# Kernel optimization log

Hardware: AMD Instinct MI355X
Metric: run time of the kernel (lower is better)

## Reference

```python
import jax, jax.numpy as jnp
import numpy as np

HEADS = 8
DIM_HEAD = 64
DIM = 128
TOPK = (8, 8, 8)  # depth, height, width


def chan_ln(x, g, b):
    # channel layernorm over axis=1 (biased variance), eps added to std
    mean = jnp.mean(x, axis=1, keepdims=True)
    var = jnp.var(x, axis=1, keepdims=True)
    return g * (x - mean) / (jnp.sqrt(var) + 1e-6) + b


def l2norm(x):
    # F.normalize(dim=1): divide by max(||x||_2, eps)
    n = jnp.sqrt(jnp.sum(x * x, axis=1, keepdims=True))
    return x / jnp.maximum(n, 1e-12)


def _forward(query_source, context, w_q, w_kv, w_out,
             ctx_gamma, ctx_beta, qs_gamma, qs_beta, out_gamma, out_beta, gamma):
    b, c, Dq, Hq, Wq = query_source.shape
    Dc, Hc, Wc = context.shape[2:]
    kd, kh, kw = TOPK

    ctx = chan_ln(context, ctx_gamma, ctx_beta)
    qs = chan_ln(query_source, qs_gamma, qs_beta)

    # 1x1x1 convs == channel matmuls
    kv = jnp.einsum('bcdhw,oc->bodhw', ctx, w_kv)   # (b, 2*inner, D, H, W)
    k, v = jnp.split(kv, 2, axis=1)
    q = jnp.einsum('bcdhw,oc->bodhw', qs, w_q)      # (b, inner, D, H, W)

    def fold(t):  # (b, h*c, D,H,W) -> (b*h, c, D,H,W)
        return t.reshape(b * HEADS, DIM_HEAD, *t.shape[2:])

    q, k, v = fold(q), fold(k), fold(v)
    q, k = l2norm(q), l2norm(k)

    q_probe = jnp.sum(q, axis=(2, 3, 4))            # (bh, c)
    k_abs = jnp.abs(k)

    if kd < Dc:
        score = jnp.einsum('bc,bcd->bd', q_probe, jnp.sum(k_abs, axis=(3, 4)))
        idx = jax.lax.top_k(score, kd)[1][:, None, :, None, None]
        k = jnp.take_along_axis(k, idx, axis=2)
        v = jnp.take_along_axis(v, idx, axis=2)
    if kh < Hc:
        score = jnp.einsum('bc,bch->bh', q_probe, jnp.sum(k_abs, axis=(2, 4)))
        idx = jax.lax.top_k(score, kh)[1][:, None, None, :, None]
        k = jnp.take_along_axis(k, idx, axis=3)
        v = jnp.take_along_axis(v, idx, axis=3)
    if kw < Wc:
        score = jnp.einsum('bc,bcw->bw', q_probe, jnp.sum(k_abs, axis=(2, 3)))
        idx = jax.lax.top_k(score, kw)[1][:, None, None, None, :]
        k = jnp.take_along_axis(k, idx, axis=4)
        v = jnp.take_along_axis(v, idx, axis=4)

    def flat(t):  # (bh, c, d, h, w) -> (bh, d*h*w, c)
        return t.reshape(t.shape[0], t.shape[1], -1).transpose(0, 2, 1)

    qf, kf, vf = flat(q), flat(k), flat(v)
    sim = jnp.einsum('bic,bjc->bij', qf, kf)        # (bh, Nq, Nkv)
    attn = jax.nn.softmax(sim, axis=-1)
    out = jnp.einsum('bij,bjc->bic', attn, vf)      # (bh, Nq, c)

    out = out.reshape(b, HEADS, Dq, Hq, Wq, DIM_HEAD)
    out = out.transpose(0, 1, 5, 2, 3, 4).reshape(b, HEADS * DIM_HEAD, Dq, Hq, Wq)
    out = jnp.einsum('bcdhw,oc->bodhw', out, w_out)
    out = chan_ln(out, out_gamma, out_beta)
    return gamma * out + query_source


def setup_inputs() -> dict:
    key = jax.random.key(0)
    ks = jax.random.split(key, 6)
    b, c, D, H, W = 2, DIM, 16, 32, 32
    inner = HEADS * DIM_HEAD
    ones = jnp.ones((1, c, 1, 1, 1), jnp.float32)
    zeros = jnp.zeros((1, c, 1, 1, 1), jnp.float32)
    return {
        'query_source': jax.random.normal(ks[0], (b, c, D, H, W), jnp.float32),
        'context': jax.random.normal(ks[1], (b, c, D, H, W), jnp.float32),
        'w_q': jax.random.normal(ks[2], (inner, c), jnp.float32) / np.sqrt(c).astype(np.float32),
        'w_kv': jax.random.normal(ks[3], (2 * inner, c), jnp.float32) / np.sqrt(c).astype(np.float32),
        'w_out': jax.random.normal(ks[4], (c, inner), jnp.float32) / np.sqrt(inner).astype(np.float32),
        'ctx_gamma': ones, 'ctx_beta': zeros,
        'qs_gamma': ones, 'qs_beta': zeros,
        'out_gamma': ones, 'out_beta': zeros,
        'gamma': jnp.full((1,), 0.5, jnp.float32),
    }


def reference(query_source, context, w_q, w_kv, w_out,
              ctx_gamma, ctx_beta, qs_gamma, qs_beta, out_gamma, out_beta, gamma):
    return _forward(query_source, context, w_q, w_kv, w_out,
                    ctx_gamma, ctx_beta, qs_gamma, qs_beta, out_gamma, out_beta, gamma)
```

## Files before the change

### kernel.cpp

```cpp
#include <hip/hip_runtime.h>
#include <hip/hip_bf16.h>

#define S_SP 16384
#define NKV 512

typedef short short8 __attribute__((ext_vector_type(8)));
typedef float v4f   __attribute__((ext_vector_type(4)));

__device__ __forceinline__ unsigned short f2bf(float x){
  union { float f; unsigned u; } v; v.f = x;
  unsigned r = v.u + 0x7FFFu + ((v.u >> 16) & 1u);
  return (unsigned short)(r >> 16);
}
__device__ __forceinline__ float bf2f(unsigned short h){
  union { unsigned u; float f; } v; v.u = ((unsigned)h) << 16; return v.f;
}

#if defined(__has_builtin)
#if __has_builtin(__builtin_amdgcn_cvt_pk_bf16_f32)
#define HAVE_PKBF 1
#endif
#endif

__device__ __forceinline__ unsigned pk2(float a, float b){
#ifdef HAVE_PKBF
  typedef __bf16 bf16x2 __attribute__((ext_vector_type(2)));
  union { bf16x2 v; unsigned u; } r;
  r.v = __builtin_amdgcn_cvt_pk_bf16_f32(a, b);
  return r.u;
#else
  return (unsigned)f2bf(a) | ((unsigned)f2bf(b) << 16);
#endif
}

__device__ __forceinline__ short8 u2s8(uint4 u){
  union { uint4 u; short8 s; } x; x.u = u; return x.s;
}

__device__ __forceinline__ void gll16(const unsigned short* g, unsigned short* l){
  __builtin_amdgcn_global_load_lds(
    (const __attribute__((address_space(1))) unsigned int*)g,
    (__attribute__((address_space(3))) unsigned int*)l, 16, 0, 0);
}

__global__ __launch_bounds__(256) void k_stats(const float* __restrict__ ctx,
                                               const float* __restrict__ qs,
                                               const float* __restrict__ ctx_g,
                                               const float* __restrict__ ctx_b,
                                               const float* __restrict__ qs_g,
                                               const float* __restrict__ qs_b,
                                               const float* __restrict__ wq,
                                               const float* __restrict__ wkv,
                                               float* __restrict__ MEAN,
                                               float* __restrict__ INV,
                                               unsigned short* __restrict__ XTC_hi,
                                               unsigned short* __restrict__ XTC_lo,
                                               unsigned short* __restrict__ XTQ_hi,
                                               unsigned short* __restrict__ XTQ_lo,
                                               unsigned short* __restrict__ WQh,
                                               unsigned short* __restrict__ WQl,
                                               unsigned short* __restrict__ WKh,
                                               unsigned short* __restrict__ WKl){
  __shared__ float r1[4][64];
  __shared__ float r2[4][64];
  __shared__ float mb[64], ib[64];
  __shared__ __align__(16) unsigned short TH[64*136];
  __shared__ __align__(16) unsigned short TL[64*136];
  int bx = blockIdx.x;
  int t = threadIdx.x;
  if (bx >= 1024){
    int wb = bx - 1024;
    int isK = wb >> 5;
    size_t i8 = ((size_t)(wb & 31)*256 + t)*8;
    const float* srcw = isK ? wkv : wq;
    unsigned short* dh = isK ? WKh : WQh;
    unsigned short* dl = isK ? WKl : WQl;
    v4f a  = *(const v4f*)(srcw + i8);
    v4f b2 = *(const v4f*)(srcw + i8 + 4);
    unsigned short h[8], l[8];
    #pragma unroll
    for (int i=0;i<4;i++){
      h[i]   = f2bf(a[i]);  l[i]   = f2bf(a[i]  - bf2f(h[i]));
      h[i+4] = f2bf(b2[i]); l[i+4] = f2bf(b2[i] - bf2f(h[i+4]));
    }
    uint4 uh, ul;
    uh.x = (unsigned)h[0] | ((unsigned)h[1]<<16);
    uh.y = (unsigned)h[2] | ((unsigned)h[3]<<16);
    uh.z = (unsigned)h[4] | ((unsigned)h[5]<<16);
    uh.w = (unsigned)h[6] | ((unsigned)h[7]<<16);
    ul.x = (unsigned)l[0] | ((unsigned)l[1]<<16);
    ul.y = (unsigned)l[2] | ((unsigned)l[3]<<16);
    ul.z = (unsigned)l[4] | ((unsigned)l[5]<<16);
    ul.w = (unsigned)l[6] | ((unsigned)l[7]<<16);
    *(uint4*)(dh + i8) = uh;
    *(uint4*)(dl + i8) = ul;
    return;
  }
  int tt = bx >> 9; int b = (bx >> 8) & 1; int sc = bx & 255;
  int sv = t & 63, cg = t >> 6;
  int s = sc*64 + sv;
  const float* src = (tt ? qs : ctx) + ((size_t)b*128 + cg*32)*S_SP + s;
  const float* G  = tt ? qs_g : ctx_g;
  const float* Bv = tt ? qs_b : ctx_b;
  float xv[32];
  float sum = 0.f, ss = 0.f;
  #pragma unroll
  for (int c = 0; c < 32; c++){
    float v = src[(size_t)c*S_SP];
    xv[c] = v;
    sum += v; ss += v*v;
  }
  r1[cg][sv] = sum; r2[cg][sv] = ss;
  __syncthreads();
  if (t < 64){
    float sm = r1[0][t]+r1[1][t]+r1[2][t]+r1[3][t];
    float sq = r2[0][t]+r2[1][t]+r2[2][t]+r2[3][t];
    float mean = sm * 0.0078125f;
    float var  = fmaxf(sq * 0.0078125f - mean*mean, 0.f);
    float inv  = 1.f/(sqrtf(var) + 1e-6f);
    int o = tt*2*S_SP + b*S_SP + sc*64 + t;
    MEAN[o] = mean; INV[o] = inv;
    mb[t] = mean; ib[t] = inv;
  }
  __syncthreads();
  float m = mb[sv], iv = ib[sv];
  #pragma unroll
  for (int i = 0; i < 32; i += 2){
    int c = cg*32 + i;
    float y0 = G[c]  *(xv[i]  -m)*iv + Bv[c];
    float y1 = G[c+1]*(xv[i+1]-m)*iv + Bv[c+1];
    unsigned short h0 = f2bf(y0), h1 = f2bf(y1);
    unsigned short l0 = f2bf(y0 - bf2f(h0)), l1 = f2bf(y1 - bf2f(h1));
    *(unsigned*)&TH[sv*136 + c] = (unsigned)h0 | ((unsigned)h1 << 16);
    *(unsigned*)&TL[sv*136 + c] = (unsigned)l0 | ((unsigned)l1 << 16);
  }
  __syncthreads();
  int row = t >> 2, seg = (t & 3) * 32;
  unsigned short* XH = tt ? XTQ_hi : XTC_hi;
  unsigned short* XL = tt ? XTQ_lo : XTC_lo;
  size_t go = ((size_t)b*S_SP + sc*64 + row)*128 + seg;
  #pragma unroll
  for (int k2 = 0; k2 < 4; k2++){
    *(uint4*)(XH + go + k2*8) = *(const uint4*)&TH[row*136 + seg + k2*8];
    *(uint4*)(XL + go + k2*8) = *(const uint4*)&TL[row*136 + seg + k2*8];
  }
}

template<int ISK>
__global__ __launch_bounds__(256) void k_proj(
    const unsigned short* __restrict__ XH, const unsigned short* __restrict__ XL,
    const unsigned short* __restrict__ WH, const unsigned short* __restrict__ WL,
    unsigned short* __restrict__ QBF, float* __restrict__ QP,
    float* __restrict__ SCORE){
  __shared__ float qpl[128];
  __shared__ float qacc[128];
  __shared__ float wacc[64];
  int bx = blockIdx.x;
  int og = bx >> 7, b = (bx >> 6) & 1, stile = bx & 63;
  int t = threadIdx.x, wvi = t >> 6, lane = t & 63;
  int quad = lane >> 4, l15 = lane & 15;
  int sw0 = stile*256 + wvi*64;
  int bh0 = b*8 + og*2;
  if (ISK){
    if (t < 128) qpl[t] = QP[bh0*64 + t];
    if (t < 64) wacc[t] = 0.f;
    __syncthreads();
  } else {
    if (t < 128) qacc[t] = 0.f;
  }
  v4f acc[8][4];
  #pragma unroll
  for (int i=0;i<8;i++)
    #pragma unroll
    for (int j=0;j<4;j++) acc[i][j] = (v4f){0.f,0.f,0.f,0.f};
  size_t wrow = ((size_t)(og*128 + l15))*128 + quad*8;
  size_t xrow = ((size_t)b*S_SP + sw0 + l15)*128 + quad*8;
  #pragma unroll 1
  for (int ks=0; ks<4; ks++){
    int ko = ks*32;
    uint4 bhv[4], blv[4], av[8];
    #pragma unroll
    for (int nt=0;nt<4;nt++){
      bhv[nt] = *(const uint4*)(XH + xrow + nt*2048 + ko);
      blv[nt] = *(const uint4*)(XL + xrow + nt*2048 + ko);
    }
    #pragma unroll
    for (int mt=0;mt<8;mt++) av[mt] = *(const uint4*)(WH + wrow + mt*2048 + ko);
    #pragma unroll
    for (int mt=0;mt<8;mt++){
      short8 am = u2s8(av[mt]);
      #pragma unroll
      for (int nt=0;nt<4;nt++)
        acc[mt][nt] = __builtin_amdgcn_mfma_f32_16x16x32_bf16(am, u2s8(bhv[nt]), acc[mt][nt], 0, 0, 0);
      #pragma unroll
      for (int nt=0;nt<4;nt++)
        acc[mt][nt] = __builtin_amdgcn_mfma_f32_16x16x32_bf16(am, u2s8(blv[nt]), acc[mt][nt], 0, 0, 0);
    }
    #pragma unroll
    for (int mt=0;mt<8;mt++){
      short8 am = u2s8(*(const uint4*)(WL + wrow + mt*2048 + ko));
      #pragma unroll
      for (int nt=0;nt<4;nt++)
        acc[mt][nt] = __builtin_amdgcn_mfma_f32_16x16x32_bf16(am, u2s8(bhv[nt]), acc[mt][nt], 0, 0, 0);
    }
  }
  float inv0[4], inv1[4];
  #pragma unroll
  for (int nt=0;nt<4;nt++){
    float p0 = 0.f, p1 = 0.f;
    #pragma unroll
    for (int mt=0;mt<4;mt++)
      #pragma unroll
      for (int r=0;r<4;r++){
        p0 += acc[mt][nt][r]*acc[mt][nt][r];
        p1 += acc[mt+4][nt][r]*acc[mt+4][nt][r];
      }
    p0 += __shfl_xor(p0,16,64); p0 += __shfl_xor(p0,32,64);
    p1 += __shfl_xor(p1,16,64); p1 += __shfl_xor(p1,32,64);
    inv0[nt] = 1.f/fmaxf(sqrtf(p0),1e-12f);
    inv1[nt] = 1.f/fmaxf(sqrtf(p1),1e-12f);
  }
  if (!ISK){
    #pragma unroll
    for (int mt=0;mt<8;mt++)
      #pragma unroll
      for (int nt=0;nt<4;nt++){
        float iv = (mt<4) ? inv0[nt] : inv1[nt];
        #pragma unroll
        for (int r=0;r<4;r++) acc[mt][nt][r] *= iv;
      }
    #pragma unroll
    for (int mt=0;mt<8;mt++){
      int bh = bh0 + (mt>>2);
      #pragma unroll
      for (int nt=0;nt<4;nt++){
        int s = sw0 + nt*16 + l15;
        uint2 wv;
        wv.x = pk2(acc[mt][nt][0], acc[mt][nt][1]);
        wv.y = pk2(acc[mt][nt][2], acc[mt][nt][3]);
        *(uint2*)(QBF + ((size_t)bh*S_SP + s)*64 + (mt&3)*16 + quad*4) = wv;
      }
    }
    __syncthreads();
    #pragma unroll
    for (int mt=0;mt<8;mt++){
      #pragma unroll
      for (int r=0;r<4;r++){
        float v = acc[mt][0][r]+acc[mt][1][r]+acc[mt][2][r]+acc[mt][3][r];
        v += __shfl_xor(v,1,64); v += __shfl_xor(v,2,64);
        v += __shfl_xor(v,4,64); v += __shfl_xor(v,8,64);
        if (l15 == 0)
          atomicAdd(&qacc[(mt>>2)*64 + (mt&3)*16 + quad*4 + r], v);
      }
    }
    __syncthreads();
    if (t < 128) atomicAdd(QP + bh0*64 + t, qacc[t]);
  } else {
    float v0[4] = {0,0,0,0}, v1[4] = {0,0,0,0};
    #pragma unroll
    for (int mt=0;mt<8;mt++){
      #pragma unroll
      for (int r=0;r<4;r++){
        float w = qpl[mt*16 + quad*4 + r];
        #pragma unroll
        for (int nt=0;nt<4;nt++){
          float av = fabsf(acc[mt][nt][r]) * w;
          if (mt < 4) v0[nt] += av; else v1[nt] += av;
        }
      }
    }
    #pragma unroll
    for (int nt=0;nt<4;nt++){
      v0[nt] += __shfl_xor(v0[nt],16,64); v0[nt] += __shfl_xor(v0[nt],32,64);
      v1[nt] += __shfl_xor(v1[nt],16,64); v1[nt] += __shfl_xor(v1[nt],32,64);
      v0[nt] *= inv0[nt]; v1[nt] *= inv1[nt];
    }
    float w00 = v0[0]+v0[2], w10 = v0[1]+v0[3];
    float w01 = v1[0]+v1[2], w11 = v1[1]+v1[3];
    float h00 = v0[0]+v0[1], h01 = v0[2]+v0[3];
    float h10 = v1[0]+v1[1], h11 = v1[2]+v1[3];
    #pragma unroll
    for (int mm=1; mm<16; mm<<=1){
      h00 += __shfl_xor(h00,mm,64); h01 += __shfl_xor(h01,mm,64);
      h10 += __shfl_xor(h10,mm,64); h11 += __shfl_xor(h11,mm,64);
    }
    if (lane < 16){
      atomicAdd(&wacc[l15],      w00);
      atomicAdd(&wacc[16+l15],   w10);
      atomicAdd(&wacc[32+l15],   w01);
      atomicAdd(&wacc[48+l15],   w11);
    }
    if (lane == 0){
      int hb = 16 + (stile&3)*8 + wvi*2;
      atomicAdd(SCORE + bh0*80 + hb,     h00);
      atomicAdd(SCORE + bh0*80 + hb + 1, h01);
      atomicAdd(SCORE + (bh0+1)*80 + hb,     h10);
      atomicAdd(SCORE + (bh0+1)*80 + hb + 1, h11);
      atomicAdd(SCORE + bh0*80 + (stile>>2), h00+h01);
      atomicAdd(SCORE + (bh0+1)*80 + (stile>>2), h10+h11);
    }
    __syncthreads();
    if (t < 64) atomicAdd(SCORE + (bh0 + (t>>5))*80 + 48 + (t&31), wacc[t]);
  }
}

__global__ __launch_bounds__(256) void k_gather(const float* __restrict__ ctx,
    const float* __restrict__ wkv, const float* __restrict__ ctx_g,
    const float* __restrict__ ctx_b, const float* __restrict__ MEAN,
    const float* __restrict__ INV, const float* __restrict__ SCORE,
    unsigned short* __restrict__ KG, unsigned short* __restrict__ VGT){
  __shared__ float wlds[64*129];
  __shared__ float xln[32*128];
  __shared__ float scb[80];
  __shared__ int sidx[24];
  int bx = blockIdx.x;
  int bh = bx >> 5, jc = (bx >> 1) & 15, type = bx & 1;
  int head = bh & 7, b = bh >> 3;
  int t = threadIdx.x;
  if (t < 80) scb[t] = SCORE[bh*80 + t];
  {
    int oc = t>>2, ks = (t&3)*32;
    const float* wr = wkv + ((size_t)(type*512 + head*64 + oc))*128 + ks;
    #pragma unroll 8
    for (int i=0;i<32;i++) wlds[oc*129 + ks + i] = wr[i];
  }
  __syncthreads();
  if (t < 64){
    #pragma unroll 1
    for (int a=0;a<3;a++){
      int n = a ? 32 : 16;
      int off = (a==0) ? 0 : (a==1 ? 16 : 48);
      float v = (t < n) ? scb[off+t] : -3.4e38f;
      #pragma unroll 1
      for (int it=0; it<8; it++){
        float bv = v; int bi = t;
        #pragma unroll
        for (int mm=1; mm<32; mm<<=1){
          float ov = __shfl_xor(bv, mm, 64);
          int oi = __shfl_xor(bi, mm, 64);
          if (ov > bv || (ov == bv && oi < bi)){ bv = ov; bi = oi; }
        }
        if (t == bi) v = -3.4e38f;
        if (t == 0) sidx[a*8+it] = bi;
      }
    }
  }
  __syncthreads();
  {
    int jl = t>>3, seg = (t&7)*16;
    int jj = jc*32 + jl;
    int dsel = sidx[jj>>6], hsel = sidx[8 + ((jj>>3)&7)], wsel = sidx[16 + (jj&7)];
    int sj = dsel*1024 + hsel*32 + wsel;
    float mn = MEAN[b*S_SP + sj];
    float iv = INV[b*S_SP + sj];
    #pragma unroll
    for (int i=0;i<16;i++){
      int cc = seg + i;
      float raw = ctx[((size_t)(b*128 + cc))*S_SP + sj];
      xln[jl*128 + cc] = ctx_g[cc]*(raw - mn)*iv + ctx_b[cc];
    }
  }
  __syncthreads();
  int c = t & 63, jg = t >> 6;
  float accv[8] = {};
  #pragma unroll 4
  for (int k=0;k<128;k++){
    float wv = wlds[c*129 + k];
    #pragma unroll
    for (int m=0;m<8;m++) accv[m] += wv * xln[(jg + 4*m)*128 + k];
  }
  #pragma unroll
  for (int m=0;m<8;m++){
    int jj = jc*32 + jg + 4*m;
    float a = accv[m];
    if (type == 0){
      float sq = a*a;
      #pragma unroll
      for (int mm=32; mm; mm>>=1) sq += __shfl_xor(sq, mm, 64);
      float rn = 1.f/fmaxf(sqrtf(sq), 1e-12f);
      KG[((size_t)bh*NKV + jj)*64 + c] = f2bf(a*rn);
    } else {
      VGT[((size_t)bh*64 + c)*NKV + jj] = f2bf(a);
    }
  }
}

__global__ __launch_bounds__(256) void k_attn(const unsigned short* __restrict__ QBF,
    const unsigned short* __restrict__ KG, const unsigned short* __restrict__ VGT,
    unsigned short* __restrict__ AOUT, int qbase){
  __shared__ __align__(16) unsigned short kst[2][64*64];
  __shared__ __align__(16) unsigned short vst[2][64*64];
  __shared__ __align__(16) unsigned short pst[4][64*36];
  int bx = blockIdx.x;
  int bh = bx >> 5, qb = qbase + (bx & 31);
  int t = threadIdx.x;
  int wvi = t >> 6, lane = t & 63;
  int quad = lane >> 4, l15 = lane & 15;
  int r3 = lane >> 3, s3 = lane & 7;
  int q0 = qb*256 + wvi*64;
  const unsigned short* kgb = KG + (size_t)bh*NKV*64;
  const unsigned short* vgb = VGT + (size_t)bh*64*NKV;
  short8 bq[4][2];
  #pragma unroll
  for (int qt=0; qt<4; qt++){
    const unsigned short* qp_ = QBF + ((size_t)bh*S_SP + q0 + qt*16 + l15)*64 + quad*8;
    union { uint4 u; short8 s; } u0, u1;
    u0.u = *(const uint4*)(qp_);
    u1.u = *(const uint4*)(qp_ + 32);
    bq[qt][0] = u0.s; bq[qt][1] = u1.s;
  }
  v4f oacc[4][4];
  #pragma unroll
  for (int i=0;i<4;i++)
    #pragma unroll
    for (int j=0;j<4;j++) oacc[i][j] = (v4f){0.f,0.f,0.f,0.f};
  float lsum[4] = {0.f,0.f,0.f,0.f};
  unsigned short* pw = pst[wvi];
  int swz = (s3 ^ r3) << 3;
  #pragma unroll
  for (int i=0;i<2;i++){
    int rowb = wvi*16 + i*8;
    gll16(kgb + ((size_t)(rowb + r3))*64 + swz,  &kst[0][rowb*64]);
    gll16(vgb + ((size_t)(rowb + r3))*NKV + swz, &vst[0][rowb*64]);
  }
  __syncthreads();
  #pragma unroll 1
  for (int ch=0; ch<8; ch++){
    int cur = ch & 1;
    if (ch < 7){
      #pragma unroll
      for (int i=0;i<2;i++){
        int rowb = wvi*16 + i*8;
        gll16(kgb + ((size_t)((ch+1)*64 + rowb + r3))*64 + swz, &kst[cur^1][rowb*64]);
        gll16(vgb + ((size_t)(rowb + r3))*NKV + (ch+1)*64 + swz, &vst[cur^1][rowb*64]);
      }
    }
    const unsigned short* kb = kst[cur];
    const unsigned short* vb = vst[cur];
    #pragma unroll
    for (int sub=0; sub<2; sub++){
      #pragma unroll
      for (int j2=0; j2<2; j2++){
        int jr = (sub*2 + j2)*16 + l15;
        int sk = jr & 7;
        union { uint4 u; short8 s; } a0, a1;
        a0.u = *(const uint4*)(kb + jr*64 + ((quad^sk)*8));
        a1.u = *(const uint4*)(kb + jr*64 + (((quad+4)^sk)*8));
        v4f s4[4];
        __builtin_amdgcn_s_setprio(1);
        #pragma unroll
        for (int qt=0; qt<4; qt++){
          v4f z = {0.f,0.f,0.f,0.f};
          z = __builtin_amdgcn_mfma_f32_16x16x32_bf16(a0.s, bq[qt][0], z, 0, 0, 0);
          z = __builtin_amdgcn_mfma_f32_16x16x32_bf16(a1.s, bq[qt][1], z, 0, 0, 0);
          s4[qt] = z;
        }
        __builtin_amdgcn_s_setprio(0);
        #pragma unroll
        for (int qt=0; qt<4; qt++){
          v4f p;
          #pragma unroll
          for (int r=0;r<4;r++) p[r] = __expf(s4[qt][r] - 1.0f);
          lsum[qt] += p[0]+p[1]+p[2]+p[3];
          uint2 wv;
          wv.x = pk2(p[0], p[1]);
          wv.y = pk2(p[2], p[3]);
          int qr = qt*16 + l15;
          *(uint2*)&pw[qr*36 + j2*16 + quad*4] = wv;
        }
      }
      short8 bp[4];
      #pragma unroll
      for (int qt=0; qt<4; qt++){
        int qr = qt*16 + l15;
        union { uint4 u; short8 s; } ub;
        ub.u = *(const uint4*)&pw[qr*36 + quad*8];
        bp[qt] = ub.s;
      }
      #pragma unroll
      for (int ct=0; ct<4; ct++){
        int cr = ct*16 + l15;
        union { uint4 u; short8 s; } av;
        av.u = *(const uint4*)(vb + cr*64 + (((sub*4+quad)^(cr&7))*8));
        __builtin_amdgcn_s_setprio(1);
        #pragma unroll
        for (int qt=0; qt<4; qt++)
          oacc[ct][qt] = __builtin_amdgcn_mfma_f32_16x16x32_bf16(av.s, bp[qt], oacc[ct][qt], 0, 0, 0);
        __builtin_amdgcn_s_setprio(0);
      }
    }
    __syncthreads();
  }
  float rl[4];
  #pragma unroll
  for (int qt=0; qt<4; qt++){
    float l = lsum[qt];
    l += __shfl_xor(l, 16, 64);
    l += __shfl_xor(l, 32, 64);
    rl[qt] = 1.f/l;
  }
  #pragma unroll
  for (int qt=0; qt<4; qt++){
    #pragma unroll
    for (int ct=0; ct<4; ct++){
      v4f o = oacc[ct][qt];
      uint2 wv;
      wv.x = pk2(o[0]*rl[qt], o[1]*rl[qt]);
      wv.y = pk2(o[2]*rl[qt], o[3]*rl[qt]);
      *(uint2*)(AOUT + ((size_t)bh*S_SP + q0 + qt*16 + l15)*64 + ct*16 + quad*4) = wv;
    }
  }
}

__global__ __launch_bounds__(256) void k_out(const unsigned short* __restrict__ AOUT,
    const float* __restrict__ wout, const float* __restrict__ out_g,
    const float* __restrict__ out_b, const float* __restrict__ gamma,
    const float* __restrict__ qsrc, float* __restrict__ OUT){
  __shared__ __align__(16) unsigned short wl[128*40];
  __shared__ float lnp[4][2][64];
  __shared__ float mbuf[64], sbuf[64], ogl[128], obl[128];
  int bx = blockIdx.x; int b = bx>>8; int stile = bx&255; int s0 = stile*64;
  int t = threadIdx.x; int w = t>>6; int lane = t&63;
  int q = lane>>4; int l15 = lane&15;
  if (t < 128){ ogl[t] = out_g[t]; obl[t] = out_b[t]; }
  v4f acc[2][4];
  #pragma unroll
  for (int i=0;i<2;i++)
    #pragma unroll
    for (int j=0;j<4;j++) acc[i][j] = (v4f){0.f,0.f,0.f,0.f};
  for (int kt=0; kt<16; kt++){
    __syncthreads();
    {
      int c = t>>1, kb = (t&1)*16;
      const float* wr = wout + (size_t)c*512 + kt*32 + kb;
      v4f a0 = *(const v4f*)wr, a1 = *(const v4f*)(wr+4);
      v4f a2 = *(const v4f*)(wr+8), a3 = *(const v4f*)(wr+12);
      uint4 u0, u1;
      u0.x = pk2(a0[0], a0[1]); u0.y = pk2(a0[2], a0[3]);
      u0.z = pk2(a1[0], a1[1]); u0.w = pk2(a1[2], a1[3]);
      u1.x = pk2(a2[0], a2[1]); u1.y = pk2(a2[2], a2[3]);
      u1.z = pk2(a3[0], a3[1]); u1.w = pk2(a3[2], a3[3]);
      *(uint4*)&wl[c*40+kb]   = u0;
      *(uint4*)&wl[c*40+kb+8] = u1;
    }
    __syncthreads();
    short8 af[2];
    #pragma unroll
    for (int mt=0;mt<2;mt++){
      union { uint4 u; short8 s; } ua;
      ua.u = *(const uint4*)&wl[(w*32+mt*16+l15)*40 + q*8];
      af[mt] = ua.s;
    }
    int head = kt>>1; int cc0 = (kt&1)*32 + q*8;
    const unsigned short* bp = AOUT + ((size_t)((b*8+head)*S_SP + s0 + l15))*64 + cc0;
    #pragma unroll
    for (int nt=0;nt<4;nt++){
      union { uint4 u; short8 s; } ub;
      ub.u = *(const uint4*)(bp + (size_t)nt*16*64);
      #pragma unroll
      for (int mt=0;mt<2;mt++)
        acc[mt][nt] = __builtin_amdgcn_mfma_f32_16x16x32_bf16(af[mt], ub.s, acc[mt][nt], 0, 0, 0);
    }
  }
  #pragma unroll
  for (int nt=0;nt<4;nt++){
    float p1 = 0.f, p2 = 0.f;
    #pragma unroll
    for (int mt=0;mt<2;mt++)
      #pragma unroll
      for (int r=0;r<4;r++){ float v = acc[mt][nt][r]; p1 += v; p2 += v*v; }
    p1 += __shfl_xor(p1,16,64); p1 += __shfl_xor(p1,32,64);
    p2 += __shfl_xor(p2,16,64); p2 += __shfl_xor(p2,32,64);
    if (q == 0){ lnp[w][0][nt*16+l15] = p1; lnp[w][1][nt*16+l15] = p2; }
  }
  __syncthreads();
  if (t < 64){
    float m = (lnp[0][0][t]+lnp[1][0][t]+lnp[2][0][t]+lnp[3][0][t]) * 0.0078125f;
    float qq = (lnp[0][1][t]+lnp[1][1][t]+lnp[2][1][t]+lnp[3][1][t]) * 0.0078125f;
    float var = fmaxf(qq - m*m, 0.f);
    mbuf[t] = m;
    sbuf[t] = 1.f/(sqrtf(var) + 1e-6f);
  }
  __syncthreads();
  float gs = gamma[0];
  #pragma unroll
  for (int nt=0;nt<4;nt++){
    int sl = nt*16 + l15;
    float mm = mbuf[sl], ssc = sbuf[sl];
    #pragma unroll
    for (int mt=0;mt<2;mt++){
      #pragma unroll
      for (int r=0;r<4;r++){
        int c = w*32 + mt*16 + q*4 + r;
        size_t adr = ((size_t)(b*128+c))*S_SP + s0 + sl;
        float yn = (acc[mt][nt][r]-mm)*ssc;
        OUT[adr] = gs*(ogl[c]*yn + obl[c]) + qsrc[adr];
      }
    }
  }
}

extern "C" void kernel_launch(void* const* d_in, const int* in_sizes, int n_in,
                              void* d_out, int out_size, void* d_ws, size_t ws_size,
                              hipStream_t stream){
  const float* qsrc  = (const float*)d_in[0];
  const float* ctx   = (const float*)d_in[1];
  const float* wq    = (const float*)d_in[2];
  const float* wkv   = (const float*)d_in[3];
  const float* wout  = (const float*)d_in[4];
  const float* ctx_g = (const float*)d_in[5];
  const float* ctx_b = (const float*)d_in[6];
  const float* qs_g  = (const float*)d_in[7];
  const float* qs_b  = (const float*)d_in[8];
  const float* out_g = (const float*)d_in[9];
  const float* out_b = (const float*)d_in[10];
  const float* gamma = (const float*)d_in[11];
  float* OUT = (float*)d_out;
  char* ws = (char*)d_ws;
  float* QP    = (float*)(ws);
  float* SCORE = (float*)(ws + 4096);
  float* MEAN  = (float*)(ws + 16384);
  float* INV   = (float*)(ws + 278528);
  unsigned short* QBF  = (unsigned short*)(ws + 544768);
  unsigned short* KG   = (unsigned short*)(ws + 34099200);
  unsigned short* VGT  = (unsigned short*)(ws + 35147776);
  unsigned short* AOUT = (unsigned short*)(ws + 36196352);
  unsigned short* WQh = (unsigned short*)(ws + 34099200);
  unsigned short* WQl = (unsigned short*)(ws + 34230272);
  unsigned short* WKh = (unsigned short*)(ws + 34361344);
  unsigned short* WKl = (unsigned short*)(ws + 34492416);
  unsigned short* XTQh = (unsigned short*)(ws + 36196352);
  unsigned short* XTQl = (unsigned short*)(ws + 44584960);
  unsigned short* XTCh = (unsigned short*)(ws + 52973568);
  unsigned short* XTCl = (unsigned short*)(ws + 61362176);

  hipMemsetAsync(ws, 0, 9216, stream);
  k_stats<<<1088, 256, 0, stream>>>(ctx, qsrc, ctx_g, ctx_b, qs_g, qs_b, wq, wkv,
                                    MEAN, INV, XTCh, XTCl, XTQh, XTQl,
                                    WQh, WQl, WKh, WKl);
  k_proj<0><<<512, 256, 0, stream>>>(XTQh, XTQl, WQh, WQl, QBF, QP, SCORE);
  k_proj<1><<<512, 256, 0, stream>>>(XTCh, XTCl, WKh, WKl, QBF, QP, SCORE);
  k_gather<<<512, 256, 0, stream>>>(ctx, wkv, ctx_g, ctx_b, MEAN, INV, SCORE, KG, VGT);
  k_attn<<<512, 256, 0, stream>>>(QBF, KG, VGT, AOUT, 0);
  k_attn<<<512, 256, 0, stream>>>(QBF, KG, VGT, AOUT, 32);
  k_out<<<512, 256, 0, stream>>>(AOUT, wout, out_g, out_b, gamma, qsrc, OUT);
}
```

Baseline: 340.4 us.

## Retile stats, projection, attention and output kernels for more blocks and overlap

```diff
diff --git a/kernel.cpp b/kernel.cpp
--- a/kernel.cpp
+++ b/kernel.cpp
@@ -6,6 +6,7 @@
 
 typedef short short8 __attribute__((ext_vector_type(8)));
 typedef float v4f   __attribute__((ext_vector_type(4)));
+typedef float v2f   __attribute__((ext_vector_type(2)));
 
 __device__ __forceinline__ unsigned short f2bf(float x){
   union { float f; unsigned u; } v; v.f = x;
@@ -61,8 +62,8 @@
                                                unsigned short* __restrict__ WQl,
                                                unsigned short* __restrict__ WKh,
                                                unsigned short* __restrict__ WKl){
-  __shared__ float r1[4][64];
-  __shared__ float r2[4][64];
+  __shared__ float r1[8][64];
+  __shared__ float r2[8][64];
   __shared__ float mb[64], ib[64];
   __shared__ __align__(16) unsigned short TH[64*136];
   __shared__ __align__(16) unsigned short TL[64*136];
@@ -97,24 +98,27 @@
     return;
   }
   int tt = bx >> 9; int b = (bx >> 8) & 1; int sc = bx & 255;
-  int sv = t & 63, cg = t >> 6;
-  int s = sc*64 + sv;
-  const float* src = (tt ? qs : ctx) + ((size_t)b*128 + cg*32)*S_SP + s;
+  int cg = t >> 5, sv2 = t & 31;
+  int s0 = sc*64;
+  const float* src = (tt ? qs : ctx) + ((size_t)(b*128 + cg*16))*S_SP + s0 + sv2*2;
   const float* G  = tt ? qs_g : ctx_g;
   const float* Bv = tt ? qs_b : ctx_b;
-  float xv[32];
-  float sum = 0.f, ss = 0.f;
-  #pragma unroll
-  for (int c = 0; c < 32; c++){
-    float v = src[(size_t)c*S_SP];
-    xv[c] = v;
-    sum += v; ss += v*v;
-  }
-  r1[cg][sv] = sum; r2[cg][sv] = ss;
+  float xa[16], xb[16];
+  float sa = 0.f, sb = 0.f, qa = 0.f, qb2 = 0.f;
+  #pragma unroll
+  for (int i = 0; i < 16; i++){
+    v2f v = *(const v2f*)(src + (size_t)i*S_SP);
+    xa[i] = v[0]; xb[i] = v[1];
+    sa += v[0]; qa += v[0]*v[0];
+    sb += v[1]; qb2 += v[1]*v[1];
+  }
+  r1[cg][sv2*2]   = sa; r1[cg][sv2*2+1] = sb;
+  r2[cg][sv2*2]   = qa; r2[cg][sv2*2+1] = qb2;
   __syncthreads();
   if (t < 64){
-    float sm = r1[0][t]+r1[1][t]+r1[2][t]+r1[3][t];
-    float sq = r2[0][t]+r2[1][t]+r2[2][t]+r2[3][t];
+    float sm = 0.f, sq = 0.f;
+    #pragma unroll
+    for (int g=0; g<8; g++){ sm += r1[g][t]; sq += r2[g][t]; }
     float mean = sm * 0.0078125f;
     float var  = fmaxf(sq * 0.0078125f - mean*mean, 0.f);
     float inv  = 1.f/(sqrtf(var) + 1e-6f);
@@ -123,16 +127,31 @@
     mb[t] = mean; ib[t] = inv;
   }
   __syncthreads();
-  float m = mb[sv], iv = ib[sv];
-  #pragma unroll
-  for (int i = 0; i < 32; i += 2){
-    int c = cg*32 + i;
-    float y0 = G[c]  *(xv[i]  -m)*iv + Bv[c];
-    float y1 = G[c+1]*(xv[i+1]-m)*iv + Bv[c+1];
-    unsigned short h0 = f2bf(y0), h1 = f2bf(y1);
-    unsigned short l0 = f2bf(y0 - bf2f(h0)), l1 = f2bf(y1 - bf2f(h1));
-    *(unsigned*)&TH[sv*136 + c] = (unsigned)h0 | ((unsigned)h1 << 16);
-    *(unsigned*)&TL[sv*136 + c] = (unsigned)l0 | ((unsigned)l1 << 16);
+  {
+    int sv = sv2*2;
+    float m = mb[sv], iv = ib[sv];
+    #pragma unroll
+    for (int i = 0; i < 16; i += 2){
+      int c = cg*16 + i;
+      float y0 = G[c]  *(xa[i]  -m)*iv + Bv[c];
+      float y1 = G[c+1]*(xa[i+1]-m)*iv + Bv[c+1];
+      unsigned short h0 = f2bf(y0), h1 = f2bf(y1);
+      unsigned short l0 = f2bf(y0 - bf2f(h0)), l1 = f2bf(y1 - bf2f(h1));
+      *(unsigned*)&TH[sv*136 + c] = (unsigned)h0 | ((unsigned)h1 << 16);
+      *(unsigned*)&TL[sv*136 + c] = (unsigned)l0 | ((unsigned)l1 << 16);
+    }
+    sv = sv2*2 + 1;
+    m = mb[sv]; iv = ib[sv];
+    #pragma unroll
+    for (int i = 0; i < 16; i += 2){
+      int c = cg*16 + i;
+      float y0 = G[c]  *(xb[i]  -m)*iv + Bv[c];
+      float y1 = G[c+1]*(xb[i+1]-m)*iv + Bv[c+1];
+      unsigned short h0 = f2bf(y0), h1 = f2bf(y1);
+      unsigned short l0 = f2bf(y0 - bf2f(h0)), l1 = f2bf(y1 - bf2f(h1));
+      *(unsigned*)&TH[sv*136 + c] = (unsigned)h0 | ((unsigned)h1 << 16);
+      *(unsigned*)&TL[sv*136 + c] = (unsigned)l0 | ((unsigned)l1 << 16);
+    }
   }
   __syncthreads();
   int row = t >> 2, seg = (t & 3) * 32;
@@ -156,10 +175,10 @@
   __shared__ float qacc[128];
   __shared__ float wacc[64];
   int bx = blockIdx.x;
-  int og = bx >> 7, b = (bx >> 6) & 1, stile = bx & 63;
+  int og = bx >> 8, b = (bx >> 7) & 1, stile = bx & 127;
   int t = threadIdx.x, wvi = t >> 6, lane = t & 63;
   int quad = lane >> 4, l15 = lane & 15;
-  int sw0 = stile*256 + wvi*64;
+  int sw0 = stile*128 + wvi*32;
   int bh0 = b*8 + og*2;
   if (ISK){
     if (t < 128) qpl[t] = QP[bh0*64 + t];
@@ -168,19 +187,19 @@
   } else {
     if (t < 128) qacc[t] = 0.f;
   }
-  v4f acc[8][4];
+  v4f acc[8][2];
   #pragma unroll
   for (int i=0;i<8;i++)
     #pragma unroll
-    for (int j=0;j<4;j++) acc[i][j] = (v4f){0.f,0.f,0.f,0.f};
+    for (int j=0;j<2;j++) acc[i][j] = (v4f){0.f,0.f,0.f,0.f};
   size_t wrow = ((size_t)(og*128 + l15))*128 + quad*8;
   size_t xrow = ((size_t)b*S_SP + sw0 + l15)*128 + quad*8;
   #pragma unroll 1
   for (int ks=0; ks<4; ks++){
     int ko = ks*32;
-    uint4 bhv[4], blv[4], av[8];
-    #pragma unroll
-    for (int nt=0;nt<4;nt++){
+    uint4 bhv[2], blv[2], av[8];
+    #pragma unroll
+    for (int nt=0;nt<2;nt++){
       bhv[nt] = *(const uint4*)(XH + xrow + nt*2048 + ko);
       blv[nt] = *(const uint4*)(XL + xrow + nt*2048 + ko);
     }
@@ -190,23 +209,23 @@
     for (int mt=0;mt<8;mt++){
       short8 am = u2s8(av[mt]);
       #pragma unroll
-      for (int nt=0;nt<4;nt++)
+      for (int nt=0;nt<2;nt++)
         acc[mt][nt] = __builtin_amdgcn_mfma_f32_16x16x32_bf16(am, u2s8(bhv[nt]), acc[mt][nt], 0, 0, 0);
       #pragma unroll
-      for (int nt=0;nt<4;nt++)
+      for (int nt=0;nt<2;nt++)
         acc[mt][nt] = __builtin_amdgcn_mfma_f32_16x16x32_bf16(am, u2s8(blv[nt]), acc[mt][nt], 0, 0, 0);
     }
     #pragma unroll
     for (int mt=0;mt<8;mt++){
       short8 am = u2s8(*(const uint4*)(WL + wrow + mt*2048 + ko));
       #pragma unroll
-      for (int nt=0;nt<4;nt++)
+      for (int nt=0;nt<2;nt++)
         acc[mt][nt] = __builtin_amdgcn_mfma_f32_16x16x32_bf16(am, u2s8(bhv[nt]), acc[mt][nt], 0, 0, 0);
     }
   }
-  float inv0[4], inv1[4];
-  #pragma unroll
-  for (int nt=0;nt<4;nt++){
+  float inv0[2], inv1[2];
+  #pragma unroll
+  for (int nt=0;nt<2;nt++){
     float p0 = 0.f, p1 = 0.f;
     #pragma unroll
     for (int mt=0;mt<4;mt++)
@@ -224,7 +243,7 @@
     #pragma unroll
     for (int mt=0;mt<8;mt++)
       #pragma unroll
-      for (int nt=0;nt<4;nt++){
+      for (int nt=0;nt<2;nt++){
         float iv = (mt<4) ? inv0[nt] : inv1[nt];
         #pragma unroll
         for (int r=0;r<4;r++) acc[mt][nt][r] *= iv;
@@ -233,7 +252,7 @@
     for (int mt=0;mt<8;mt++){
       int bh = bh0 + (mt>>2);
       #pragma unroll
-      for (int nt=0;nt<4;nt++){
+      for (int nt=0;nt<2;nt++){
         int s = sw0 + nt*16 + l15;
         uint2 wv;
         wv.x = pk2(acc[mt][nt][0], acc[mt][nt][1]);
@@ -246,7 +265,7 @@
     for (int mt=0;mt<8;mt++){
       #pragma unroll
       for (int r=0;r<4;r++){
-        float v = acc[mt][0][r]+acc[mt][1][r]+acc[mt][2][r]+acc[mt][3][r];
+        float v = acc[mt][0][r]+acc[mt][1][r];
         v += __shfl_xor(v,1,64); v += __shfl_xor(v,2,64);
         v += __shfl_xor(v,4,64); v += __shfl_xor(v,8,64);
         if (l15 == 0)
@@ -256,48 +275,43 @@
     __syncthreads();
     if (t < 128) atomicAdd(QP + bh0*64 + t, qacc[t]);
   } else {
-    float v0[4] = {0,0,0,0}, v1[4] = {0,0,0,0};
+    float v0[2] = {0.f,0.f}, v1[2] = {0.f,0.f};
     #pragma unroll
     for (int mt=0;mt<8;mt++){
       #pragma unroll
       for (int r=0;r<4;r++){
         float w = qpl[mt*16 + quad*4 + r];
         #pragma unroll
-        for (int nt=0;nt<4;nt++){
+        for (int nt=0;nt<2;nt++){
           float av = fabsf(acc[mt][nt][r]) * w;
           if (mt < 4) v0[nt] += av; else v1[nt] += av;
         }
       }
     }
     #pragma unroll
-    for (int nt=0;nt<4;nt++){
+    for (int nt=0;nt<2;nt++){
       v0[nt] += __shfl_xor(v0[nt],16,64); v0[nt] += __shfl_xor(v0[nt],32,64);
       v1[nt] += __shfl_xor(v1[nt],16,64); v1[nt] += __shfl_xor(v1[nt],32,64);
       v0[nt] *= inv0[nt]; v1[nt] *= inv1[nt];
     }
-    float w00 = v0[0]+v0[2], w10 = v0[1]+v0[3];
-    float w01 = v1[0]+v1[2], w11 = v1[1]+v1[3];
-    float h00 = v0[0]+v0[1], h01 = v0[2]+v0[3];
-    float h10 = v1[0]+v1[1], h11 = v1[2]+v1[3];
+    if (lane < 16){
+      atomicAdd(&wacc[l15],      v0[0]);
+      atomicAdd(&wacc[16+l15],   v0[1]);
+      atomicAdd(&wacc[32+l15],   v1[0]);
+      atomicAdd(&wacc[48+l15],   v1[1]);
+    }
+    float h0 = v0[0] + v0[1], h1 = v1[0] + v1[1];
     #pragma unroll
     for (int mm=1; mm<16; mm<<=1){
-      h00 += __shfl_xor(h00,mm,64); h01 += __shfl_xor(h01,mm,64);
-      h10 += __shfl_xor(h10,mm,64); h11 += __shfl_xor(h11,mm,64);
-    }
-    if (lane < 16){
-      atomicAdd(&wacc[l15],      w00);
-      atomicAdd(&wacc[16+l15],   w10);
-      atomicAdd(&wacc[32+l15],   w01);
-      atomicAdd(&wacc[48+l15],   w11);
+      h0 += __shfl_xor(h0,mm,64); h1 += __shfl_xor(h1,mm,64);
     }
     if (lane == 0){
-      int hb = 16 + (stile&3)*8 + wvi*2;
-      atomicAdd(SCORE + bh0*80 + hb,     h00);
-      atomicAdd(SCORE + bh0*80 + hb + 1, h01);
-      atomicAdd(SCORE + (bh0+1)*80 + hb,     h10);
-      atomicAdd(SCORE + (bh0+1)*80 + hb + 1, h11);
-      atomicAdd(SCORE + bh0*80 + (stile>>2), h00+h01);
-      atomicAdd(SCORE + (bh0+1)*80 + (stile>>2), h10+h11);
+      int hh = 16 + (stile&7)*4 + wvi;
+      int dd = stile >> 3;
+      atomicAdd(SCORE + bh0*80 + hh, h0);
+      atomicAdd(SCORE + (bh0+1)*80 + hh, h1);
+      atomicAdd(SCORE + bh0*80 + dd, h0);
+      atomicAdd(SCORE + (bh0+1)*80 + dd, h1);
     }
     __syncthreads();
     if (t < 64) atomicAdd(SCORE + (bh0 + (t>>5))*80 + 48 + (t&31), wacc[t]);
@@ -387,12 +401,12 @@
 
 __global__ __launch_bounds__(256) void k_attn(const unsigned short* __restrict__ QBF,
     const unsigned short* __restrict__ KG, const unsigned short* __restrict__ VGT,
-    unsigned short* __restrict__ AOUT, int qbase){
+    unsigned short* __restrict__ AOUT){
   __shared__ __align__(16) unsigned short kst[2][64*64];
   __shared__ __align__(16) unsigned short vst[2][64*64];
   __shared__ __align__(16) unsigned short pst[4][64*36];
   int bx = blockIdx.x;
-  int bh = bx >> 5, qb = qbase + (bx & 31);
+  int bh = bx >> 6, qb = bx & 63;
   int t = threadIdx.x;
   int wvi = t >> 6, lane = t & 63;
   int quad = lane >> 4, l15 = lane & 15;
@@ -516,23 +530,35 @@
     const float* __restrict__ wout, const float* __restrict__ out_g,
     const float* __restrict__ out_b, const float* __restrict__ gamma,
     const float* __restrict__ qsrc, float* __restrict__ OUT){
-  __shared__ __align__(16) unsigned short wl[128*40];
+  __shared__ __align__(16) unsigned short wl[2][128*40];
   __shared__ float lnp[4][2][64];
   __shared__ float mbuf[64], sbuf[64], ogl[128], obl[128];
   int bx = blockIdx.x; int b = bx>>8; int stile = bx&255; int s0 = stile*64;
   int t = threadIdx.x; int w = t>>6; int lane = t&63;
   int q = lane>>4; int l15 = lane&15;
   if (t < 128){ ogl[t] = out_g[t]; obl[t] = out_b[t]; }
+  int cst = t>>1, kbs = (t&1)*16;
   v4f acc[2][4];
   #pragma unroll
   for (int i=0;i<2;i++)
     #pragma unroll
     for (int j=0;j<4;j++) acc[i][j] = (v4f){0.f,0.f,0.f,0.f};
+  {
+    const float* wr = wout + (size_t)cst*512 + kbs;
+    v4f a0 = *(const v4f*)wr, a1 = *(const v4f*)(wr+4);
+    v4f a2 = *(const v4f*)(wr+8), a3 = *(const v4f*)(wr+12);
+    uint4 u0, u1;
+    u0.x = pk2(a0[0], a0[1]); u0.y = pk2(a0[2], a0[3]);
+    u0.z = pk2(a1[0], a1[1]); u0.w = pk2(a1[2], a1[3]);
+    u1.x = pk2(a2[0], a2[1]); u1.y = pk2(a2[2], a2[3]);
+    u1.z = pk2(a3[0], a3[1]); u1.w = pk2(a3[2], a3[3]);
+    *(uint4*)&wl[0][cst*40+kbs]   = u0;
+    *(uint4*)&wl[0][cst*40+kbs+8] = u1;
+  }
+  __syncthreads();
   for (int kt=0; kt<16; kt++){
-    __syncthreads();
-    {
-      int c = t>>1, kb = (t&1)*16;
-      const float* wr = wout + (size_t)c*512 + kt*32 + kb;
+    if (kt < 15){
+      const float* wr = wout + (size_t)cst*512 + (kt+1)*32 + kbs;
       v4f a0 = *(const v4f*)wr, a1 = *(const v4f*)(wr+4);
       v4f a2 = *(const v4f*)(wr+8), a3 = *(const v4f*)(wr+12);
       uint4 u0, u1;
@@ -540,15 +566,15 @@
       u0.z = pk2(a1[0], a1[1]); u0.w = pk2(a1[2], a1[3]);
       u1.x = pk2(a2[0], a2[1]); u1.y = pk2(a2[2], a2[3]);
       u1.z = pk2(a3[0], a3[1]); u1.w = pk2(a3[2], a3[3]);
-      *(uint4*)&wl[c*40+kb]   = u0;
-      *(uint4*)&wl[c*40+kb+8] = u1;
-    }
-    __syncthreads();
+      *(uint4*)&wl[(kt+1)&1][cst*40+kbs]   = u0;
+      *(uint4*)&wl[(kt+1)&1][cst*40+kbs+8] = u1;
+    }
+    const unsigned short* wb = wl[kt&1];
     short8 af[2];
     #pragma unroll
     for (int mt=0;mt<2;mt++){
       union { uint4 u; short8 s; } ua;
-      ua.u = *(const uint4*)&wl[(w*32+mt*16+l15)*40 + q*8];
+      ua.u = *(const uint4*)&wb[(w*32+mt*16+l15)*40 + q*8];
       af[mt] = ua.s;
     }
     int head = kt>>1; int cc0 = (kt&1)*32 + q*8;
@@ -561,6 +587,7 @@
       for (int mt=0;mt<2;mt++)
         acc[mt][nt] = __builtin_amdgcn_mfma_f32_16x16x32_bf16(af[mt], ub.s, acc[mt][nt], 0, 0, 0);
     }
+    __syncthreads();
   }
   #pragma unroll
   for (int nt=0;nt<4;nt++){
@@ -638,10 +665,9 @@
   k_stats<<<1088, 256, 0, stream>>>(ctx, qsrc, ctx_g, ctx_b, qs_g, qs_b, wq, wkv,
                                     MEAN, INV, XTCh, XTCl, XTQh, XTQl,
                                     WQh, WQl, WKh, WKl);
-  k_proj<0><<<512, 256, 0, stream>>>(XTQh, XTQl, WQh, WQl, QBF, QP, SCORE);
-  k_proj<1><<<512, 256, 0, stream>>>(XTCh, XTCl, WKh, WKl, QBF, QP, SCORE);
+  k_proj<0><<<1024, 256, 0, stream>>>(XTQh, XTQl, WQh, WQl, QBF, QP, SCORE);
+  k_proj<1><<<1024, 256, 0, stream>>>(XTCh, XTCl, WKh, WKl, QBF, QP, SCORE);
   k_gather<<<512, 256, 0, stream>>>(ctx, wkv, ctx_g, ctx_b, MEAN, INV, SCORE, KG, VGT);
-  k_attn<<<512, 256, 0, stream>>>(QBF, KG, VGT, AOUT, 0);
-  k_attn<<<512, 256, 0, stream>>>(QBF, KG, VGT, AOUT, 32);
+  k_attn<<<1024, 256, 0, stream>>>(QBF, KG, VGT, AOUT);
   k_out<<<512, 256, 0, stream>>>(AOUT, wout, out_g, out_b, gamma, qsrc, OUT);
 }
```

Result: slower. 361.5 us (+6.2%).
